# Optimization experiments

Measured on AMD Instinct MI355X. Metric: run time of the kernel, lower is better.

## Reference

```python
import jax, jax.numpy as jnp
import numpy as np

N, LMAX, D, VOCAB, CVOCAB = 50000, 12, 512, 1552, 80


def setup_inputs() -> dict:
    key = jax.random.key(0)
    ks = jax.random.split(key, 8)
    return {
        "word_ids": jax.random.randint(ks[0], (N,), 0, VOCAB),
        "char_ids": jax.random.randint(ks[1], (N, LMAX), 0, CVOCAB),
        "char_lens": jax.random.randint(ks[2], (N,), 1, LMAX + 1),
        "word_embed_table": jax.random.normal(ks[3], (VOCAB, D), jnp.float32) * 0.02,
        "char_embed_table": jax.random.normal(ks[4], (CVOCAB, D), jnp.float32) * 0.02,
        "char_proj_w": jax.random.normal(ks[5], (D,), jnp.float32) * 0.04,
        "char_proj_b": jnp.zeros((1,), jnp.float32),
        "word_proj_w": jax.random.normal(ks[6], (D,), jnp.float32) * 0.04,
        "word_proj_b": jnp.zeros((1,), jnp.float32),
        "clf_w": jax.random.normal(ks[7], (VOCAB, D), jnp.float32) * 0.04,
        "clf_b": jnp.zeros((VOCAB,), jnp.float32),
    }


def reference(word_ids, char_ids, char_lens, word_embed_table, char_embed_table,
              char_proj_w, char_proj_b, word_proj_w, word_proj_b, clf_w, clf_b):
    # word embedding lookup: [N, D]
    we = word_embed_table[word_ids]
    # char embedding lookup (padded): [N, L, D]
    ce = char_embed_table[char_ids]
    # char_proj = Linear(512, 1): scores per char, [N, L]
    pre = jnp.einsum("nld,d->nl", ce, char_proj_w) + char_proj_b
    # mask out padding (reproduces the ragged per-word loop of the original)
    mask = (jnp.arange(LMAX) < char_lens[:, None]).astype(pre.dtype)  # [N, L]
    # attn_weights = pre_attn^T @ word_char_embed per word -> [N, D]
    char_pool = jnp.einsum("nl,nld->nd", pre * mask, ce)
    # all_embed = sigmoid(word_embed * char_embed): [N, D]
    all_embed = jax.nn.sigmoid(we * char_pool)
    # word_proj = Linear(512, 1) + Swish(beta=1): [N]
    wa = jnp.einsum("nd,d->n", all_embed, word_proj_w) + word_proj_b
    wa = wa * jax.nn.sigmoid(wa)
    # word_weights = word_attn^T @ all_embed: [1, D]
    word_weights = jnp.einsum("n,nd->d", wa, all_embed)[None, :]
    # classifier Linear(512, 1552): [1, VOCAB]
    res = word_weights @ clf_w.T + clf_b
    return (all_embed, res)
```

## Files before the change

kernel.cpp:

```cpp
#include <hip/hip_runtime.h>
#include <math.h>

#define LMAXC 12
#define DIM   512
#define VOC   1552
#define NCHAR 80
#define SCALE     4096.0f
#define INV_SCALE (1.0f/4096.0f)

typedef float vf4 __attribute__((ext_vector_type(4)));
typedef float vf2 __attribute__((ext_vector_type(2)));
typedef unsigned short ushort_t;

#define WW8_OFF 0
#define U_OFF   4096
#define U_BYTE_OFF 16384
#define WT_OFF  14464

__device__ __forceinline__ float sigmoidf_fast(float x) {
    return 1.0f / (1.0f + __expf(-x));
}

__device__ __forceinline__ ushort_t f2bf(float f) {
    unsigned u = __float_as_uint(f);
    u = (u + 0x7fffu + ((u >> 16) & 1u)) >> 16;
    return (ushort_t)u;
}

__device__ __forceinline__ float wave_sum_bcast(float x) {
    float s = x;
    s += __int_as_float(__builtin_amdgcn_update_dpp(0, __float_as_int(s), 0x111, 0xf, 0xf, true));
    s += __int_as_float(__builtin_amdgcn_update_dpp(0, __float_as_int(s), 0x112, 0xf, 0xf, true));
    s += __int_as_float(__builtin_amdgcn_update_dpp(0, __float_as_int(s), 0x114, 0xf, 0xf, true));
    s += __int_as_float(__builtin_amdgcn_update_dpp(0, __float_as_int(s), 0x118, 0xf, 0xf, true));
    s += __int_as_float(__builtin_amdgcn_update_dpp(0, __float_as_int(s), 0x142, 0xf, 0xf, true));
    s += __int_as_float(__builtin_amdgcn_update_dpp(0, __float_as_int(s), 0x143, 0xf, 0xf, true));
    return __int_as_float(__builtin_amdgcn_readlane(__float_as_int(s), 63));
}

#if __has_builtin(__builtin_amdgcn_cvt_pk_fp8_f32) && __has_builtin(__builtin_amdgcn_cvt_pk_f32_fp8)
#define HW_FP8 1
#else
#define HW_FP8 0
#endif

#if !HW_FP8
__device__ __forceinline__ unsigned char f2fp8_sw(float f) {
    unsigned u = __float_as_uint(f);
    unsigned s = (u >> 24) & 0x80u;
    float a = fabsf(f);
    if (a < 0.015625f) return (unsigned char)s;
    if (a > 448.f) a = 448.f;
    u = __float_as_uint(a);
    u = u + 0x7ffffu + ((u >> 20) & 1u);
    int e8 = (int)(u >> 23) - 120;
    if (e8 <= 0) return (unsigned char)s;
    if (e8 > 15) e8 = 15;
    return (unsigned char)(s | (e8 << 3) | ((u >> 20) & 7u));
}
__device__ __forceinline__ float fp8_to_f32_sw(unsigned b) {
    unsigned e = (b >> 3) & 15u, m = b & 7u, s = (b & 0x80u) << 24;
    if (e == 0) return __uint_as_float(s);
    return __uint_as_float(s | ((e + 120u) << 23) | (m << 20));
}
#endif

__device__ __forceinline__ ushort_t pack2_fp8(float f0, float f1) {
#if HW_FP8
    return (ushort_t)(__builtin_amdgcn_cvt_pk_fp8_f32(f0, f1, 0, false) & 0xffffu);
#else
    return (ushort_t)(f2fp8_sw(f0) | ((unsigned)f2fp8_sw(f1) << 8));
#endif
}

__global__ __launch_bounds__(256)
void setup_kernel(const float* __restrict__ ctab,
                  const float* __restrict__ cpw,
                  const float* __restrict__ cpb,
                  const float* __restrict__ wtab,
                  float*       __restrict__ ws)
{
    __shared__ float red[4];
    const int b   = blockIdx.x;
    const int tid = threadIdx.x;
    unsigned char* u8 = (unsigned char*)ws + U_BYTE_OFF;

    if (b < NCHAR) {
        const float a0 = ctab[b * DIM + 2 * tid];
        const float a1 = ctab[b * DIM + 2 * tid + 1];
        float p = a0 * cpw[2 * tid] + a1 * cpw[2 * tid + 1];
        #pragma unroll
        for (int off = 32; off > 0; off >>= 1) p += __shfl_xor(p, off, 64);
        if ((tid & 63) == 0) red[tid >> 6] = p;
        __syncthreads();
        const float s = (red[0] + red[1] + red[2] + red[3] + cpb[0]) * SCALE;
        ((ushort_t*)u8)[b * 256 + tid] = pack2_fp8(s * a0, s * a1);
    } else if (b == NCHAR) {
        for (int i = tid; i < 8 * DIM; i += 256) ws[WW8_OFF + i] = 0.f;
        if (tid < 128) ((unsigned int*)(u8 + NCHAR * DIM))[tid] = 0u;
    } else {
        const int r0 = (b - NCHAR - 1) * 4;
        ushort_t* wt16 = (ushort_t*)(ws + WT_OFF);
        #pragma unroll
        for (int i = 0; i < 8; ++i) {
            const int idx = r0 * DIM + i * 256 + tid;
            wt16[idx] = f2bf(wtab[idx] * INV_SCALE);
        }
    }
}

__device__ __forceinline__ void bf8_unpack(uint4 v, float* f) {
    f[0] = __uint_as_float(v.x << 16); f[1] = __uint_as_float(v.x & 0xffff0000u);
    f[2] = __uint_as_float(v.y << 16); f[3] = __uint_as_float(v.y & 0xffff0000u);
    f[4] = __uint_as_float(v.z << 16); f[5] = __uint_as_float(v.z & 0xffff0000u);
    f[6] = __uint_as_float(v.w << 16); f[7] = __uint_as_float(v.w & 0xffff0000u);
}

__global__ __launch_bounds__(512)
void fused_word_kernel(const int*   __restrict__ word_ids,
                       const int*   __restrict__ char_ids,
                       const int*   __restrict__ char_lens,
                       const float* __restrict__ wpw,
                       const float* __restrict__ wpb,
                       const float* __restrict__ ws,
                       float*       __restrict__ all_embed,
                       float*       __restrict__ ww8,
                       int n)
{
    __shared__ __align__(16) unsigned char smem[41472];

    {
        const uint4* src = (const uint4*)((const unsigned char*)ws + U_BYTE_OFF);
        uint4* dst = (uint4*)smem;
        for (int i = threadIdx.x; i < 2592; i += 512) dst[i] = src[i];
    }
    __syncthreads();

    const int lane = threadIdx.x & 63;
    const int wv   = threadIdx.x >> 6;
    const int d0   = lane << 3;
    const ushort_t* wt16 = (const ushort_t*)(ws + WT_OFF);

    const vf4 pw0 = *(const vf4*)(wpw + d0);
    const vf4 pw1 = *(const vf4*)(wpw + d0 + 4);
    const float wb = wpb[0];

    vf4 acc0 = {0.f, 0.f, 0.f, 0.f};
    vf4 acc1 = {0.f, 0.f, 0.f, 0.f};

    const int gw0     = (blockIdx.x << 3) + wv;
    const int gstride = gridDim.x << 3;

    int wu = 0, len = 0;
    int4 ci0 = {0,0,0,0}, ci1 = ci0, ci2 = ci0;
    uint4 wvec = {0,0,0,0};

    int w = gw0;
    if (w < n) {
        wu  = __builtin_amdgcn_readfirstlane(w);
        const int wid = word_ids[wu];
        len = char_lens[wu];
        const int4* cp = (const int4*)(char_ids + (size_t)wu * LMAXC);
        ci0 = cp[0]; ci1 = cp[1]; ci2 = cp[2];
        wvec = *(const uint4*)(wt16 + (size_t)wid * DIM + d0);
    }

    while (w < n) {
        const int wn   = w + gstride;
        const int wun  = __builtin_amdgcn_readfirstlane(wn < n ? wn : 0);
        const int widn = word_ids[wun];
        const int lenn = char_lens[wun];
        const int4* cpn = (const int4*)(char_ids + (size_t)wun * LMAXC);
        const int4 m0 = cpn[0], m1 = cpn[1], m2 = cpn[2];
        const uint4 wvecn = *(const uint4*)(wt16 + (size_t)widn * DIM + d0);

        const int cid[LMAXC] = {ci0.x, ci0.y, ci0.z, ci0.w,
                                ci1.x, ci1.y, ci1.z, ci1.w,
                                ci2.x, ci2.y, ci2.z, ci2.w};
        int cide[LMAXC];
        #pragma unroll
        for (int l = 0; l < LMAXC; ++l) cide[l] = (l < len) ? cid[l] : NCHAR;

        vf2 q0 = {0.f, 0.f}, q1 = q0, q2 = q0, q3 = q0;
        #pragma unroll
        for (int l = 0; l < LMAXC; ++l) {
            const uint2 rv = *(const uint2*)(smem + cide[l] * DIM + (lane << 3));
#if HW_FP8
            q0 += __builtin_amdgcn_cvt_pk_f32_fp8((int)rv.x, false);
            q1 += __builtin_amdgcn_cvt_pk_f32_fp8((int)rv.x, true);
            q2 += __builtin_amdgcn_cvt_pk_f32_fp8((int)rv.y, false);
            q3 += __builtin_amdgcn_cvt_pk_f32_fp8((int)rv.y, true);
#else
            q0.x += fp8_to_f32_sw(rv.x & 0xffu);        q0.y += fp8_to_f32_sw((rv.x >> 8) & 0xffu);
            q1.x += fp8_to_f32_sw((rv.x >> 16) & 0xffu); q1.y += fp8_to_f32_sw(rv.x >> 24);
            q2.x += fp8_to_f32_sw(rv.y & 0xffu);        q2.y += fp8_to_f32_sw((rv.y >> 8) & 0xffu);
            q3.x += fp8_to_f32_sw((rv.y >> 16) & 0xffu); q3.y += fp8_to_f32_sw(rv.y >> 24);
#endif
        }
        const float p[8] = {q0.x, q0.y, q1.x, q1.y, q2.x, q2.y, q3.x, q3.y};

        float we[8];
        bf8_unpack(wvec, we);
        float ae[8];
        #pragma unroll
        for (int j = 0; j < 8; ++j) ae[j] = sigmoidf_fast(we[j] * p[j]);

        const vf4 a0v = {ae[0], ae[1], ae[2], ae[3]};
        const vf4 a1v = {ae[4], ae[5], ae[6], ae[7]};

        float* op = all_embed + (size_t)wu * DIM + d0;
        __builtin_nontemporal_store(a0v, (vf4*)op);
        __builtin_nontemporal_store(a1v, (vf4*)(op + 4));

        const float sdot = ae[0]*pw0.x + ae[1]*pw0.y + ae[2]*pw0.z + ae[3]*pw0.w
                         + ae[4]*pw1.x + ae[5]*pw1.y + ae[6]*pw1.z + ae[7]*pw1.w;
        const float tot = wave_sum_bcast(sdot);
        float wa = tot + wb;
        wa = wa * sigmoidf_fast(wa);

        acc0 += wa * a0v;
        acc1 += wa * a1v;

        w = wn; wu = wun; len = lenn;
        ci0 = m0; ci1 = m1; ci2 = m2; wvec = wvecn;
    }

    __syncthreads();
    float* red = (float*)smem;
    *(vf4*)(red + wv * DIM + d0)     = acc0;
    *(vf4*)(red + wv * DIM + d0 + 4) = acc1;
    __syncthreads();

    const int slice = blockIdx.x & 7;
    for (int d = threadIdx.x; d < DIM; d += 512) {
        float s = 0.f;
        #pragma unroll
        for (int k = 0; k < 8; ++k) s += red[k * DIM + d];
        atomicAdd(ww8 + slice * DIM + d, s);
    }
}

__global__ __launch_bounds__(256)
void clf_kernel(const float* __restrict__ ww8,
                const float* __restrict__ clf_w,
                const float* __restrict__ clf_b,
                float*       __restrict__ res)
{
    const int lane = threadIdx.x & 63;
    const int wv   = threadIdx.x >> 6;
    const int v    = (blockIdx.x << 2) + wv;
    if (v >= VOC) return;

    const int d0 = lane << 3;
    float w[8];
    #pragma unroll
    for (int j = 0; j < 8; ++j) w[j] = 0.f;
    #pragma unroll
    for (int s = 0; s < 8; ++s) {
        const float4 a = *(const float4*)(ww8 + s * DIM + d0);
        const float4 b = *(const float4*)(ww8 + s * DIM + d0 + 4);
        w[0] += a.x; w[1] += a.y; w[2] += a.z; w[3] += a.w;
        w[4] += b.x; w[5] += b.y; w[6] += b.z; w[7] += b.w;
    }

    const float* cr = clf_w + (size_t)v * DIM + d0;
    const float4 a0 = *(const float4*)(cr);
    const float4 a1 = *(const float4*)(cr + 4);
    const float p = w[0]*a0.x + w[1]*a0.y + w[2]*a0.z + w[3]*a0.w
                  + w[4]*a1.x + w[5]*a1.y + w[6]*a1.z + w[7]*a1.w;
    const float tot = wave_sum_bcast(p);
    if (lane == 0) res[v] = tot + clf_b[v];
}

extern "C" void kernel_launch(void* const* d_in, const int* in_sizes, int n_in,
                              void* d_out, int out_size, void* d_ws, size_t ws_size,
                              hipStream_t stream) {
    const int*   word_ids  = (const int*)  d_in[0];
    const int*   char_ids  = (const int*)  d_in[1];
    const int*   char_lens = (const int*)  d_in[2];
    const float* wtab      = (const float*)d_in[3];
    const float* ctab      = (const float*)d_in[4];
    const float* cpw       = (const float*)d_in[5];
    const float* cpb       = (const float*)d_in[6];
    const float* wpw       = (const float*)d_in[7];
    const float* wpb       = (const float*)d_in[8];
    const float* clf_w     = (const float*)d_in[9];
    const float* clf_b     = (const float*)d_in[10];

    const int n = in_sizes[0];
    float* out       = (float*)d_out;
    float* all_embed = out;
    float* res       = out + (size_t)n * DIM;
    float* ws        = (float*)d_ws;

    setup_kernel<<<NCHAR + 1 + (VOC / 4), 256, 0, stream>>>(ctab, cpw, cpb, wtab, ws);

    fused_word_kernel<<<1024, 512, 0, stream>>>(
        word_ids, char_ids, char_lens,
        wpw, wpb, ws, all_embed, ws + WW8_OFF, n);

    clf_kernel<<<(VOC + 3) / 4, 256, 0, stream>>>(ws + WW8_OFF, clf_w, clf_b, res);
}
```

Baseline: 44.40 us.

## Read char rows from global/L2 with two-deep software pipeline instead of LDS staging

Drops the per-block copy of the fp8 char-score table into shared memory and gathers the rows straight from global memory (L2-resident). The loop now processes two words per iteration, with row gathers and scalar index loads issued two and four words ahead to hide the latency. Blocks shrink to 256 threads and the grid doubles, so the final reduction sums four waves. The gathers now have global-memory latency instead of LDS latency, and holding 24 prefetched rows per lane adds register pressure.

```diff
diff --git a/kernel.cpp b/kernel.cpp
--- a/kernel.cpp
+++ b/kernel.cpp
@@ -13,7 +13,6 @@
 typedef unsigned short ushort_t;
 
 #define WW8_OFF 0
-#define U_OFF   4096
 #define U_BYTE_OFF 16384
 #define WT_OFF  14464
 
@@ -116,7 +115,79 @@
     f[6] = __uint_as_float(v.w << 16); f[7] = __uint_as_float(v.w & 0xffff0000u);
 }
 
-__global__ __launch_bounds__(512)
+struct WScal { int4 a, b, c; int wid; int len; };
+
+__device__ __forceinline__ void load_scal(WScal& s, int wc,
+                                          const int* __restrict__ word_ids,
+                                          const int* __restrict__ char_lens,
+                                          const int* __restrict__ char_ids) {
+    s.wid = word_ids[wc];
+    s.len = char_lens[wc];
+    const int4* cp = (const int4*)(char_ids + (size_t)wc * LMAXC);
+    s.a = cp[0]; s.b = cp[1]; s.c = cp[2];
+}
+
+__device__ __forceinline__ void issue_rows(uint2 (&r)[LMAXC], const WScal& s,
+                                           const unsigned char* __restrict__ u8, int d8) {
+    const int ids[LMAXC] = {s.a.x, s.a.y, s.a.z, s.a.w,
+                            s.b.x, s.b.y, s.b.z, s.b.w,
+                            s.c.x, s.c.y, s.c.z, s.c.w};
+    #pragma unroll
+    for (int l = 0; l < LMAXC; ++l) {
+        const int cc = (l < s.len) ? ids[l] : NCHAR;
+        r[l] = *(const uint2*)(u8 + cc * DIM + d8);
+    }
+}
+
+__device__ __forceinline__ void do_word(const uint2 (&r)[LMAXC], uint4 wvec, int w, bool valid,
+                                        vf4 pw0, vf4 pw1, float wb,
+                                        float* __restrict__ all_embed, int d0,
+                                        vf4& acc0, vf4& acc1)
+{
+    vf2 q0 = {0.f, 0.f}, q1 = q0, q2 = q0, q3 = q0;
+    #pragma unroll
+    for (int l = 0; l < LMAXC; ++l) {
+#if HW_FP8
+        q0 += __builtin_amdgcn_cvt_pk_f32_fp8((int)r[l].x, false);
+        q1 += __builtin_amdgcn_cvt_pk_f32_fp8((int)r[l].x, true);
+        q2 += __builtin_amdgcn_cvt_pk_f32_fp8((int)r[l].y, false);
+        q3 += __builtin_amdgcn_cvt_pk_f32_fp8((int)r[l].y, true);
+#else
+        q0.x += fp8_to_f32_sw(r[l].x & 0xffu);         q0.y += fp8_to_f32_sw((r[l].x >> 8) & 0xffu);
+        q1.x += fp8_to_f32_sw((r[l].x >> 16) & 0xffu); q1.y += fp8_to_f32_sw(r[l].x >> 24);
+        q2.x += fp8_to_f32_sw(r[l].y & 0xffu);         q2.y += fp8_to_f32_sw((r[l].y >> 8) & 0xffu);
+        q3.x += fp8_to_f32_sw((r[l].y >> 16) & 0xffu); q3.y += fp8_to_f32_sw(r[l].y >> 24);
+#endif
+    }
+    const float p[8] = {q0.x, q0.y, q1.x, q1.y, q2.x, q2.y, q3.x, q3.y};
+
+    float we[8];
+    bf8_unpack(wvec, we);
+    float ae[8];
+    #pragma unroll
+    for (int j = 0; j < 8; ++j) ae[j] = sigmoidf_fast(we[j] * p[j]);
+
+    const vf4 a0v = {ae[0], ae[1], ae[2], ae[3]};
+    const vf4 a1v = {ae[4], ae[5], ae[6], ae[7]};
+
+    if (valid) {
+        float* op = all_embed + (size_t)w * DIM + d0;
+        __builtin_nontemporal_store(a0v, (vf4*)op);
+        __builtin_nontemporal_store(a1v, (vf4*)(op + 4));
+    }
+
+    const float sdot = ae[0]*pw0.x + ae[1]*pw0.y + ae[2]*pw0.z + ae[3]*pw0.w
+                     + ae[4]*pw1.x + ae[5]*pw1.y + ae[6]*pw1.z + ae[7]*pw1.w;
+    const float tot = wave_sum_bcast(sdot);
+    float wa = tot + wb;
+    wa = wa * sigmoidf_fast(wa);
+    if (!valid) wa = 0.f;
+
+    acc0 += wa * a0v;
+    acc1 += wa * a1v;
+}
+
+__global__ __launch_bounds__(256)
 void fused_word_kernel(const int*   __restrict__ word_ids,
                        const int*   __restrict__ char_ids,
                        const int*   __restrict__ char_lens,
@@ -127,115 +198,66 @@
                        float*       __restrict__ ww8,
                        int n)
 {
-    __shared__ __align__(16) unsigned char smem[41472];
-
-    {
-        const uint4* src = (const uint4*)((const unsigned char*)ws + U_BYTE_OFF);
-        uint4* dst = (uint4*)smem;
-        for (int i = threadIdx.x; i < 2592; i += 512) dst[i] = src[i];
-    }
-    __syncthreads();
-
     const int lane = threadIdx.x & 63;
     const int wv   = threadIdx.x >> 6;
     const int d0   = lane << 3;
+    const unsigned char* u8 = (const unsigned char*)ws + U_BYTE_OFF;
     const ushort_t* wt16 = (const ushort_t*)(ws + WT_OFF);
 
     const vf4 pw0 = *(const vf4*)(wpw + d0);
     const vf4 pw1 = *(const vf4*)(wpw + d0 + 4);
     const float wb = wpb[0];
 
-    vf4 acc0 = {0.f, 0.f, 0.f, 0.f};
-    vf4 acc1 = {0.f, 0.f, 0.f, 0.f};
-
-    const int gw0     = (blockIdx.x << 3) + wv;
-    const int gstride = gridDim.x << 3;
-
-    int wu = 0, len = 0;
-    int4 ci0 = {0,0,0,0}, ci1 = ci0, ci2 = ci0;
-    uint4 wvec = {0,0,0,0};
-
-    int w = gw0;
-    if (w < n) {
-        wu  = __builtin_amdgcn_readfirstlane(w);
-        const int wid = word_ids[wu];
-        len = char_lens[wu];
-        const int4* cp = (const int4*)(char_ids + (size_t)wu * LMAXC);
-        ci0 = cp[0]; ci1 = cp[1]; ci2 = cp[2];
-        wvec = *(const uint4*)(wt16 + (size_t)wid * DIM + d0);
+    vf4 acc0 = {0.f, 0.f, 0.f, 0.f}, acc1 = acc0;
+
+    const int g = gridDim.x << 2;
+    int w = (blockIdx.x << 2) + wv;
+
+    WScal S2, S3;
+    uint2 rA[LMAXC], rB[LMAXC];
+    uint4 wvA, wvB;
+
+    {
+        WScal S0, S1;
+        load_scal(S0, (w         < n) ? w         : 0, word_ids, char_lens, char_ids);
+        load_scal(S1, (w + g     < n) ? w + g     : 0, word_ids, char_lens, char_ids);
+        load_scal(S2, (w + 2*g   < n) ? w + 2*g   : 0, word_ids, char_lens, char_ids);
+        load_scal(S3, (w + 3*g   < n) ? w + 3*g   : 0, word_ids, char_lens, char_ids);
+        issue_rows(rA, S0, u8, d0);
+        wvA = *(const uint4*)(wt16 + (size_t)S0.wid * DIM + d0);
+        issue_rows(rB, S1, u8, d0);
+        wvB = *(const uint4*)(wt16 + (size_t)S1.wid * DIM + d0);
     }
 
     while (w < n) {
-        const int wn   = w + gstride;
-        const int wun  = __builtin_amdgcn_readfirstlane(wn < n ? wn : 0);
-        const int widn = word_ids[wun];
-        const int lenn = char_lens[wun];
-        const int4* cpn = (const int4*)(char_ids + (size_t)wun * LMAXC);
-        const int4 m0 = cpn[0], m1 = cpn[1], m2 = cpn[2];
-        const uint4 wvecn = *(const uint4*)(wt16 + (size_t)widn * DIM + d0);
-
-        const int cid[LMAXC] = {ci0.x, ci0.y, ci0.z, ci0.w,
-                                ci1.x, ci1.y, ci1.z, ci1.w,
-                                ci2.x, ci2.y, ci2.z, ci2.w};
-        int cide[LMAXC];
-        #pragma unroll
-        for (int l = 0; l < LMAXC; ++l) cide[l] = (l < len) ? cid[l] : NCHAR;
-
-        vf2 q0 = {0.f, 0.f}, q1 = q0, q2 = q0, q3 = q0;
-        #pragma unroll
-        for (int l = 0; l < LMAXC; ++l) {
-            const uint2 rv = *(const uint2*)(smem + cide[l] * DIM + (lane << 3));
-#if HW_FP8
-            q0 += __builtin_amdgcn_cvt_pk_f32_fp8((int)rv.x, false);
-            q1 += __builtin_amdgcn_cvt_pk_f32_fp8((int)rv.x, true);
-            q2 += __builtin_amdgcn_cvt_pk_f32_fp8((int)rv.y, false);
-            q3 += __builtin_amdgcn_cvt_pk_f32_fp8((int)rv.y, true);
-#else
-            q0.x += fp8_to_f32_sw(rv.x & 0xffu);        q0.y += fp8_to_f32_sw((rv.x >> 8) & 0xffu);
-            q1.x += fp8_to_f32_sw((rv.x >> 16) & 0xffu); q1.y += fp8_to_f32_sw(rv.x >> 24);
-            q2.x += fp8_to_f32_sw(rv.y & 0xffu);        q2.y += fp8_to_f32_sw((rv.y >> 8) & 0xffu);
-            q3.x += fp8_to_f32_sw((rv.y >> 16) & 0xffu); q3.y += fp8_to_f32_sw(rv.y >> 24);
-#endif
+        do_word(rA, wvA, w, true, pw0, pw1, wb, all_embed, d0, acc0, acc1);
+        issue_rows(rA, S2, u8, d0);
+        wvA = *(const uint4*)(wt16 + (size_t)S2.wid * DIM + d0);
+        {
+            const int wp = w + 4*g;
+            load_scal(S2, (wp < n) ? wp : 0, word_ids, char_lens, char_ids);
         }
-        const float p[8] = {q0.x, q0.y, q1.x, q1.y, q2.x, q2.y, q3.x, q3.y};
-
-        float we[8];
-        bf8_unpack(wvec, we);
-        float ae[8];
-        #pragma unroll
-        for (int j = 0; j < 8; ++j) ae[j] = sigmoidf_fast(we[j] * p[j]);
-
-        const vf4 a0v = {ae[0], ae[1], ae[2], ae[3]};
-        const vf4 a1v = {ae[4], ae[5], ae[6], ae[7]};
-
-        float* op = all_embed + (size_t)wu * DIM + d0;
-        __builtin_nontemporal_store(a0v, (vf4*)op);
-        __builtin_nontemporal_store(a1v, (vf4*)(op + 4));
-
-        const float sdot = ae[0]*pw0.x + ae[1]*pw0.y + ae[2]*pw0.z + ae[3]*pw0.w
-                         + ae[4]*pw1.x + ae[5]*pw1.y + ae[6]*pw1.z + ae[7]*pw1.w;
-        const float tot = wave_sum_bcast(sdot);
-        float wa = tot + wb;
-        wa = wa * sigmoidf_fast(wa);
-
-        acc0 += wa * a0v;
-        acc1 += wa * a1v;
-
-        w = wn; wu = wun; len = lenn;
-        ci0 = m0; ci1 = m1; ci2 = m2; wvec = wvecn;
-    }
-
+
+        const int w1 = w + g;
+        do_word(rB, wvB, w1, w1 < n, pw0, pw1, wb, all_embed, d0, acc0, acc1);
+        issue_rows(rB, S3, u8, d0);
+        wvB = *(const uint4*)(wt16 + (size_t)S3.wid * DIM + d0);
+        {
+            const int wp = w1 + 4*g;
+            load_scal(S3, (wp < n) ? wp : 0, word_ids, char_lens, char_ids);
+        }
+
+        w += 2*g;
+    }
+
+    __shared__ __align__(16) float red[4][DIM];
+    *(vf4*)&red[wv][d0]     = acc0;
+    *(vf4*)&red[wv][d0 + 4] = acc1;
     __syncthreads();
-    float* red = (float*)smem;
-    *(vf4*)(red + wv * DIM + d0)     = acc0;
-    *(vf4*)(red + wv * DIM + d0 + 4) = acc1;
-    __syncthreads();
 
     const int slice = blockIdx.x & 7;
-    for (int d = threadIdx.x; d < DIM; d += 512) {
-        float s = 0.f;
-        #pragma unroll
-        for (int k = 0; k < 8; ++k) s += red[k * DIM + d];
+    for (int d = threadIdx.x; d < DIM; d += 256) {
+        const float s = red[0][d] + red[1][d] + red[2][d] + red[3][d];
         atomicAdd(ww8 + slice * DIM + d, s);
     }
 }
@@ -295,7 +317,7 @@
 
     setup_kernel<<<NCHAR + 1 + (VOC / 4), 256, 0, stream>>>(ctab, cpw, cpb, wtab, ws);
 
-    fused_word_kernel<<<1024, 512, 0, stream>>>(
+    fused_word_kernel<<<2048, 256, 0, stream>>>(
         word_ids, char_ids, char_lens,
         wpw, wpb, ws, all_embed, ws + WW8_OFF, n);
 
```

New measurement: 52.55 us. +18.4%, slower.
